# Kernel tuning notes

Hardware: AMD Instinct MI355X
Metric: run time of the kernel (lower is better)

## Reference

```python
import jax, jax.numpy as jnp
import numpy as np

IN_F, OUT_F, K, BATCH = 1024, 1024, 8, 4096


def setup_inputs() -> dict:
    key = jax.random.key(0)
    kx, ka, kb = jax.random.split(key, 3)
    x = jax.random.normal(kx, (BATCH, IN_F), dtype=jnp.float32)
    scale = 1.0 / (K * OUT_F)
    # a/b params: uniform in (-1,1)/(K*out_features), laid out [out, in, K]
    a = (2.0 * jax.random.uniform(ka, (OUT_F, IN_F, K)) - 1.0) * scale
    b = (2.0 * jax.random.uniform(kb, (OUT_F, IN_F, K)) - 1.0) * scale
    return {"x": x, "a": a.astype(jnp.float32), "b": b.astype(jnp.float32)}


def reference(x, a, b):
    # Fourier basis: k = 0..K-1 applied to every input feature
    K_ = a.shape[-1]
    ks = jnp.arange(K_, dtype=x.dtype)  # [K]
    phase = x[..., None] * ks  # [B, in, K]
    x_sin = jnp.sin(phase)
    x_cos = jnp.cos(phase)
    # y[b,o] = sum_{i,k} sin(k x_bi) a_oik + cos(k x_bi) b_oik
    y = jnp.einsum("bik,oik->bo", x_sin, a) + jnp.einsum("bik,oik->bo", x_cos, b)
    return y
```

## Files before the change

kernel.cpp:

```cpp
#include <hip/hip_runtime.h>

#define BATCH   4096
#define IN_F    1024
#define OUT_F   1024
#define KF      8
#define KD      14336

#define BM 256
#define BN 256
#define BK 64
#define KSPLIT 4
#define KCHUNK (KD/KSPLIT)
#define NT (KCHUNK/BK)
#define C_ELEMS ((size_t)BATCH * OUT_F)

#define QW 1040384.0f
#define DQ (1.0f/132128768.0f)

typedef int   i32x4 __attribute__((ext_vector_type(4)));
typedef float f32x4 __attribute__((ext_vector_type(4)));

__device__ __forceinline__ void gload_lds16(const void* g, void* l) {
  __builtin_amdgcn_global_load_lds((const __attribute__((address_space(1))) void*)g,
                                   (__attribute__((address_space(3))) void*)l,
                                   16, 0, 0);
}

__device__ __forceinline__ unsigned int pack4(int q0, int q1, int q2, int q3) {
  return (unsigned int)(q0 & 255) | ((unsigned int)(q1 & 255) << 8) |
         ((unsigned int)(q2 & 255) << 16) | ((unsigned int)(q3 & 255) << 24);
}

__global__ __launch_bounds__(256) void wconv_kernel(const float* __restrict__ a,
                                                    const float* __restrict__ b,
                                                    signed char* __restrict__ W,
                                                    float* __restrict__ bias) {
  const int o  = blockIdx.x;
  const int i0 = threadIdx.x * 4;
  const float4* ap = reinterpret_cast<const float4*>(a + (size_t)o * 8192 + i0 * 8);
  const float4* bp = reinterpret_cast<const float4*>(b + (size_t)o * 8192 + i0 * 8);
  union { float4 v[2]; float f[8]; } ua[4], ub[4];
#pragma unroll
  for (int ii = 0; ii < 4; ++ii) {
    ua[ii].v[0] = ap[2 * ii]; ua[ii].v[1] = ap[2 * ii + 1];
    ub[ii].v[0] = bp[2 * ii]; ub[ii].v[1] = bp[2 * ii + 1];
  }
  unsigned int* wp = reinterpret_cast<unsigned int*>(W + (size_t)o * KD + i0);
#pragma unroll
  for (int j = 0; j < 7; ++j) {
    int qa[4], qb[4];
#pragma unroll
    for (int ii = 0; ii < 4; ++ii) {
      qa[ii] = __float2int_rn(ua[ii].f[j + 1] * QW);
      qb[ii] = __float2int_rn(ub[ii].f[j + 1] * QW);
    }
    wp[j       * (IN_F / 4)] = pack4(qa[0], qa[1], qa[2], qa[3]);
    wp[(7 + j) * (IN_F / 4)] = pack4(qb[0], qb[1], qb[2], qb[3]);
  }
  float bsum = ub[0].f[0] + ub[1].f[0] + ub[2].f[0] + ub[3].f[0];
#pragma unroll
  for (int off = 32; off > 0; off >>= 1) bsum += __shfl_down(bsum, off);
  __shared__ float red[4];
  if ((threadIdx.x & 63) == 0) red[threadIdx.x >> 6] = bsum;
  __syncthreads();
  if (threadIdx.x == 0) bias[o] = red[0] + red[1] + red[2] + red[3];
}

__global__ __launch_bounds__(256) void feat_kernel(const float* __restrict__ x,
                                                   signed char* __restrict__ Xq) {
  int idx = blockIdx.x * 256 + threadIdx.x;
  int bb = idx >> 8;
  int i0 = (idx & 255) * 4;
  float4 xv = *reinterpret_cast<const float4*>(x + (size_t)bb * IN_F + i0);
  float sv[4][KF], cv[4][KF];
#pragma unroll
  for (int ii = 0; ii < 4; ++ii) {
    float xx = (ii == 0) ? xv.x : (ii == 1) ? xv.y : (ii == 2) ? xv.z : xv.w;
    sincosf(xx, &sv[ii][1], &cv[ii][1]);
#pragma unroll
    for (int k = 2; k < KF; ++k) {
      sv[ii][k] = sv[ii][k-1] * cv[ii][1] + cv[ii][k-1] * sv[ii][1];
      cv[ii][k] = cv[ii][k-1] * cv[ii][1] - sv[ii][k-1] * sv[ii][1];
    }
  }
  unsigned int* dst = reinterpret_cast<unsigned int*>(Xq + (size_t)bb * KD + i0);
#pragma unroll
  for (int j = 0; j < 7; ++j) {
    dst[j * (IN_F / 4)] = pack4(__float2int_rn(127.f * sv[0][j+1]), __float2int_rn(127.f * sv[1][j+1]),
                                __float2int_rn(127.f * sv[2][j+1]), __float2int_rn(127.f * sv[3][j+1]));
    dst[(7 + j) * (IN_F / 4)] = pack4(__float2int_rn(127.f * cv[0][j+1]), __float2int_rn(127.f * cv[1][j+1]),
                                      __float2int_rn(127.f * cv[2][j+1]), __float2int_rn(127.f * cv[3][j+1]));
  }
}

__global__ __launch_bounds__(512, 2) void gemm_kernel(const signed char* __restrict__ A,
                                                      const signed char* __restrict__ Bt,
                                                      int* __restrict__ Cout,
                                                      int use_slab) {
  __shared__ signed char sA[2][BM * BK];
  __shared__ signed char sB[2][BN * BK];

  const int tid  = threadIdx.x;
  const int wid  = tid >> 6;
  const int lane = tid & 63;
  const int wm = wid >> 2, wn = wid & 3;
  const int l15 = lane & 15;

  const int bid = blockIdx.x;
  const int s   = (bid & 7) * 32 + (bid >> 3);
  const int z   = s >> 6;
  const int mt  = s & 15;
  const int nt  = (s >> 4) & 3;
  const int m0  = mt * BM;
  const int n0  = nt * BN;
  const int fbase = z * KCHUNK;

  const int srow = wid * 16 + (lane >> 2);
  const int swz  = ((lane >> 2) & 3) ^ ((lane >> 4) & 3);
  const int gsrc = (lane & 3) ^ swz;
  const signed char* pA = A  + (size_t)(m0 + srow) * KD + fbase + gsrc * 16;
  const signed char* pB = Bt + (size_t)(n0 + srow) * KD + fbase + gsrc * 16;
  const int ldst = wid * 1024;

  const int rswz = (l15 & 3) ^ ((l15 >> 2) & 3);
  const int kgr  = (((lane >> 4) ^ rswz) & 3) * 16;
  const int arowb = (wm * 128 + l15) * BK;
  const int browb = (wn * 64 + l15) * BK;

  i32x4 acc[8][4] = {};
  i32x4 bfr[4];

#define PHASE(SAC, SBC, Q, STGP, STGDST, KOFF)                                  \
  {                                                                             \
    i32x4 af[4];                                                                \
    _Pragma("unroll") for (int f = 0; f < 4; ++f)                               \
      af[f] = *reinterpret_cast<const i32x4*>(                                  \
          (SAC) + arowb + ((Q) * 4 + f) * (16 * BK) + kgr);                     \
    if ((Q) == 0) {                                                             \
      _Pragma("unroll") for (int nf = 0; nf < 4; ++nf)                          \
        bfr[nf] = *reinterpret_cast<const i32x4*>(                              \
            (SBC) + browb + nf * (16 * BK) + kgr);                              \
    }                                                                           \
    gload_lds16((STGP) + (KOFF), (STGDST) + ldst);                              \
    gload_lds16((STGP) + (size_t)128 * KD + (KOFF), (STGDST) + 8192 + ldst);    \
    if ((Q) == 0) asm volatile("s_waitcnt lgkmcnt(4)" ::: "memory");            \
    asm volatile("s_barrier" ::: "memory");                                     \
    __builtin_amdgcn_s_setprio(1);                                              \
    _Pragma("unroll") for (int f = 0; f < 4; ++f)                               \
      _Pragma("unroll") for (int nf = 0; nf < 4; ++nf)                          \
        acc[(Q) * 4 + f][nf] = __builtin_amdgcn_mfma_i32_16x16x64_i8(           \
            af[f], bfr[nf], acc[(Q) * 4 + f][nf], 0, 0, 0);                     \
    __builtin_amdgcn_s_setprio(0);                                              \
    if ((Q) == 1) asm volatile("s_waitcnt vmcnt(2)" ::: "memory");              \
    asm volatile("s_barrier" ::: "memory");                                     \
  }

  gload_lds16(pA,                        &sA[0][ldst]);
  gload_lds16(pA + (size_t)128 * KD,     &sA[0][8192 + ldst]);
  gload_lds16(pB,                        &sB[0][ldst]);
  gload_lds16(pB + (size_t)128 * KD,     &sB[0][8192 + ldst]);
  gload_lds16(pB + BK,                   &sB[1][ldst]);
  gload_lds16(pB + (size_t)128 * KD + BK, &sB[1][8192 + ldst]);
  asm volatile("s_waitcnt vmcnt(2)" ::: "memory");
  asm volatile("s_barrier" ::: "memory");

  for (int j = 0; j < NT / 2; ++j) {
    const int kA1 = (2 * j + 1) * BK;
    const int kB2 = (2 * j + 2 < NT) ? (2 * j + 2) * BK : 0;
    const int kB3 = (2 * j + 3 < NT) ? (2 * j + 3) * BK : 0;

    PHASE(&sA[0][0], &sB[0][0], 0, pA, &sA[1][0], kA1)
    PHASE(&sA[0][0], &sB[0][0], 1, pB, &sB[0][0], kB2)
    PHASE(&sA[1][0], &sB[1][0], 0, pA, &sA[0][0], kB2)
    PHASE(&sA[1][0], &sB[1][0], 1, pB, &sB[1][0], kB3)
  }
#undef PHASE

  const int crow = m0 + wm * 128 + (lane >> 4) * 4;
  const int ccol = n0 + wn * 64 + l15;
  if (use_slab) {
    int* Cz = Cout + (size_t)z * C_ELEMS;
#pragma unroll
    for (int mf = 0; mf < 8; ++mf)
#pragma unroll
      for (int nf = 0; nf < 4; ++nf)
#pragma unroll
        for (int jj = 0; jj < 4; ++jj)
          Cz[(size_t)(crow + mf * 16 + jj) * OUT_F + ccol + nf * 16] = acc[mf][nf][jj];
  } else {
    float* Cf = reinterpret_cast<float*>(Cout);
#pragma unroll
    for (int mf = 0; mf < 8; ++mf)
#pragma unroll
      for (int nf = 0; nf < 4; ++nf)
#pragma unroll
        for (int jj = 0; jj < 4; ++jj)
          atomicAdd(&Cf[(size_t)(crow + mf * 16 + jj) * OUT_F + ccol + nf * 16],
                    (float)acc[mf][nf][jj] * DQ);
  }
}

__global__ __launch_bounds__(256) void reduce_kernel(const i32x4* __restrict__ s,
                                                     const float* __restrict__ bias,
                                                     f32x4* __restrict__ y) {
  size_t i = (size_t)blockIdx.x * 256 + threadIdx.x;
  const size_t NQ = C_ELEMS / 4;
  i32x4 v = s[i] + s[i + NQ] + s[i + 2 * NQ] + s[i + 3 * NQ];
  f32x4 bv = reinterpret_cast<const f32x4*>(bias)[i & 255];
  f32x4 r;
  r[0] = (float)v[0] * DQ + bv[0];
  r[1] = (float)v[1] * DQ + bv[1];
  r[2] = (float)v[2] * DQ + bv[2];
  r[3] = (float)v[3] * DQ + bv[3];
  y[i] = r;
}

__global__ __launch_bounds__(256) void binit_kernel(const float* __restrict__ bias,
                                                    f32x4* __restrict__ y) {
  size_t i = (size_t)blockIdx.x * 256 + threadIdx.x;
  y[i] = reinterpret_cast<const f32x4*>(bias)[i & 255];
}

__global__ __launch_bounds__(256) void naive_kernel(const float* __restrict__ x,
                                                    const float* __restrict__ a,
                                                    const float* __restrict__ b,
                                                    float* __restrict__ y) {
  int o  = blockIdx.x * 256 + threadIdx.x;
  int bb = blockIdx.y;
  __shared__ float xs[IN_F];
  for (int i = threadIdx.x; i < IN_F; i += 256) xs[i] = x[(size_t)bb * IN_F + i];
  __syncthreads();
  float acc = 0.f;
  for (int i = 0; i < IN_F; ++i) {
    float s1, c1; sincosf(xs[i], &s1, &c1);
    float sk = 0.f, ck = 1.f;
    const float* ap = a + (size_t)o * 8192 + i * KF;
    const float* bp = b + (size_t)o * 8192 + i * KF;
#pragma unroll
    for (int k = 0; k < KF; ++k) {
      acc += sk * ap[k] + ck * bp[k];
      float sn = sk * c1 + ck * s1;
      ck = ck * c1 - sk * s1;
      sk = sn;
    }
  }
  y[(size_t)bb * OUT_F + o] = acc;
}

extern "C" void kernel_launch(void* const* d_in, const int* in_sizes, int n_in,
                              void* d_out, int out_size, void* d_ws, size_t ws_size,
                              hipStream_t stream) {
  (void)in_sizes; (void)n_in; (void)out_size;
  const float* x = (const float*)d_in[0];
  const float* a = (const float*)d_in[1];
  const float* b = (const float*)d_in[2];
  float* y = (float*)d_out;

  const size_t XQ_BYTES   = (size_t)BATCH * KD;
  const size_t WQ_BYTES   = (size_t)OUT_F * KD;
  const size_t BIAS_BYTES = (size_t)OUT_F * sizeof(float);
  const size_t SLAB_BYTES = C_ELEMS * sizeof(int) * KSPLIT;

  if (ws_size >= XQ_BYTES + WQ_BYTES + BIAS_BYTES) {
    signed char* Xq = (signed char*)d_ws;
    signed char* Wq = (signed char*)d_ws + XQ_BYTES;
    float* bias     = (float*)((char*)d_ws + XQ_BYTES + WQ_BYTES);
    int* slabs      = (int*)((char*)d_ws + XQ_BYTES + WQ_BYTES + BIAS_BYTES);
    const bool slab = ws_size >= XQ_BYTES + WQ_BYTES + BIAS_BYTES + SLAB_BYTES;

    wconv_kernel<<<OUT_F, 256, 0, stream>>>(a, b, Wq, bias);
    feat_kernel<<<(BATCH * IN_F / 4) / 256, 256, 0, stream>>>(x, Xq);
    if (slab) {
      gemm_kernel<<<dim3((BATCH / BM) * (OUT_F / BN) * KSPLIT), 512, 0, stream>>>(Xq, Wq, slabs, 1);
      reduce_kernel<<<(int)(C_ELEMS / 4 / 256), 256, 0, stream>>>((const i32x4*)slabs, bias, (f32x4*)y);
    } else {
      binit_kernel<<<(int)(C_ELEMS / 4 / 256), 256, 0, stream>>>(bias, (f32x4*)y);
      gemm_kernel<<<dim3((BATCH / BM) * (OUT_F / BN) * KSPLIT), 512, 0, stream>>>(Xq, Wq, (int*)y, 0);
    }
  } else {
    naive_kernel<<<dim3(OUT_F / 256, BATCH), 256, 0, stream>>>(x, a, b, y);
  }
}
```

Measured before the change: 118.3 us.

## Load B fragments directly from global into registers, drop B LDS staging

Removes the shared-memory double buffer for the B operand. Each wave now loads its B fragments straight from global memory into registers, double-buffered across tiles. Only A is staged through LDS, which halves LDS traffic and footprint and changes the barrier schedule. The cost is that B fragments are no longer shared across the two M-waves that use them, so redundant global/L2 reads go up. Global latency is also exposed on the register path, and the __syncthreads at the end of each tile adds serialization.

Result: slower. 132.2 us (+11.7%).

```diff
diff --git a/kernel.cpp b/kernel.cpp
--- a/kernel.cpp
+++ b/kernel.cpp
@@ -98,7 +98,6 @@
                                                       int* __restrict__ Cout,
                                                       int use_slab) {
   __shared__ signed char sA[2][BM * BK];
-  __shared__ signed char sB[2][BN * BK];
 
   const int tid  = threadIdx.x;
   const int wid  = tid >> 6;
@@ -118,63 +117,65 @@
   const int srow = wid * 16 + (lane >> 2);
   const int swz  = ((lane >> 2) & 3) ^ ((lane >> 4) & 3);
   const int gsrc = (lane & 3) ^ swz;
-  const signed char* pA = A  + (size_t)(m0 + srow) * KD + fbase + gsrc * 16;
-  const signed char* pB = Bt + (size_t)(n0 + srow) * KD + fbase + gsrc * 16;
+  const signed char* pA = A + (size_t)(m0 + srow) * KD + fbase + gsrc * 16;
   const int ldst = wid * 1024;
 
   const int rswz = (l15 & 3) ^ ((l15 >> 2) & 3);
   const int kgr  = (((lane >> 4) ^ rswz) & 3) * 16;
   const int arowb = (wm * 128 + l15) * BK;
-  const int browb = (wn * 64 + l15) * BK;
+
+  const signed char* pBf = Bt + (size_t)(n0 + wn * 64 + l15) * KD + fbase + (lane >> 4) * 16;
 
   i32x4 acc[8][4] = {};
-  i32x4 bfr[4];
-
-#define PHASE(SAC, SBC, Q, STGP, STGDST, KOFF)                                  \
-  {                                                                             \
-    i32x4 af[4];                                                                \
-    _Pragma("unroll") for (int f = 0; f < 4; ++f)                               \
-      af[f] = *reinterpret_cast<const i32x4*>(                                  \
-          (SAC) + arowb + ((Q) * 4 + f) * (16 * BK) + kgr);                     \
-    if ((Q) == 0) {                                                             \
-      _Pragma("unroll") for (int nf = 0; nf < 4; ++nf)                          \
-        bfr[nf] = *reinterpret_cast<const i32x4*>(                              \
-            (SBC) + browb + nf * (16 * BK) + kgr);                              \
-    }                                                                           \
-    gload_lds16((STGP) + (KOFF), (STGDST) + ldst);                              \
-    gload_lds16((STGP) + (size_t)128 * KD + (KOFF), (STGDST) + 8192 + ldst);    \
-    if ((Q) == 0) asm volatile("s_waitcnt lgkmcnt(4)" ::: "memory");            \
-    asm volatile("s_barrier" ::: "memory");                                     \
-    __builtin_amdgcn_s_setprio(1);                                              \
-    _Pragma("unroll") for (int f = 0; f < 4; ++f)                               \
-      _Pragma("unroll") for (int nf = 0; nf < 4; ++nf)                          \
-        acc[(Q) * 4 + f][nf] = __builtin_amdgcn_mfma_i32_16x16x64_i8(           \
-            af[f], bfr[nf], acc[(Q) * 4 + f][nf], 0, 0, 0);                     \
-    __builtin_amdgcn_s_setprio(0);                                              \
-    if ((Q) == 1) asm volatile("s_waitcnt vmcnt(2)" ::: "memory");              \
-    asm volatile("s_barrier" ::: "memory");                                     \
-  }
-
-  gload_lds16(pA,                        &sA[0][ldst]);
-  gload_lds16(pA + (size_t)128 * KD,     &sA[0][8192 + ldst]);
-  gload_lds16(pB,                        &sB[0][ldst]);
-  gload_lds16(pB + (size_t)128 * KD,     &sB[0][8192 + ldst]);
-  gload_lds16(pB + BK,                   &sB[1][ldst]);
-  gload_lds16(pB + (size_t)128 * KD + BK, &sB[1][8192 + ldst]);
-  asm volatile("s_waitcnt vmcnt(2)" ::: "memory");
-  asm volatile("s_barrier" ::: "memory");
+  i32x4 BA[4], BB[4];
+
+#define TILE(SAC, SAN, BC, BN_, KOFF)                                          \
+  {                                                                            \
+    gload_lds16(pA + (KOFF), (SAN) + ldst);                                    \
+    gload_lds16(pA + (size_t)128 * KD + (KOFF), (SAN) + 8192 + ldst);          \
+    _Pragma("unroll") for (int nf = 0; nf < 4; ++nf)                           \
+      BN_[nf] = *reinterpret_cast<const i32x4*>(                               \
+          pBf + (size_t)nf * 16 * KD + (KOFF));                                \
+    __builtin_amdgcn_sched_barrier(0);                                         \
+    i32x4 af[8];                                                               \
+    _Pragma("unroll") for (int f = 0; f < 4; ++f)                              \
+      af[f] = *reinterpret_cast<const i32x4*>(                                 \
+          (SAC) + arowb + f * (16 * BK) + kgr);                                \
+    asm volatile("s_barrier" ::: "memory");                                    \
+    __builtin_amdgcn_s_setprio(1);                                             \
+    _Pragma("unroll") for (int f = 0; f < 4; ++f)                              \
+      _Pragma("unroll") for (int nf = 0; nf < 4; ++nf)                         \
+        acc[f][nf] = __builtin_amdgcn_mfma_i32_16x16x64_i8(                    \
+            af[f], BC[nf], acc[f][nf], 0, 0, 0);                               \
+    __builtin_amdgcn_s_setprio(0);                                             \
+    asm volatile("s_barrier" ::: "memory");                                    \
+    _Pragma("unroll") for (int f = 4; f < 8; ++f)                              \
+      af[f] = *reinterpret_cast<const i32x4*>(                                 \
+          (SAC) + arowb + f * (16 * BK) + kgr);                                \
+    asm volatile("s_barrier" ::: "memory");                                    \
+    __builtin_amdgcn_s_setprio(1);                                             \
+    _Pragma("unroll") for (int f = 4; f < 8; ++f)                              \
+      _Pragma("unroll") for (int nf = 0; nf < 4; ++nf)                         \
+        acc[f][nf] = __builtin_amdgcn_mfma_i32_16x16x64_i8(                    \
+            af[f], BC[nf], acc[f][nf], 0, 0, 0);                               \
+    __builtin_amdgcn_s_setprio(0);                                             \
+    __syncthreads();                                                           \
+  }
+
+  gload_lds16(pA, &sA[0][ldst]);
+  gload_lds16(pA + (size_t)128 * KD, &sA[0][8192 + ldst]);
+#pragma unroll
+  for (int nf = 0; nf < 4; ++nf)
+    BA[nf] = *reinterpret_cast<const i32x4*>(pBf + (size_t)nf * 16 * KD);
+  __syncthreads();
 
   for (int j = 0; j < NT / 2; ++j) {
-    const int kA1 = (2 * j + 1) * BK;
-    const int kB2 = (2 * j + 2 < NT) ? (2 * j + 2) * BK : 0;
-    const int kB3 = (2 * j + 3 < NT) ? (2 * j + 3) * BK : 0;
-
-    PHASE(&sA[0][0], &sB[0][0], 0, pA, &sA[1][0], kA1)
-    PHASE(&sA[0][0], &sB[0][0], 1, pB, &sB[0][0], kB2)
-    PHASE(&sA[1][0], &sB[1][0], 0, pA, &sA[0][0], kB2)
-    PHASE(&sA[1][0], &sB[1][0], 1, pB, &sB[1][0], kB3)
-  }
-#undef PHASE
+    const int k1 = (2 * j + 1) * BK;
+    const int k2 = (2 * j + 2 < NT) ? (2 * j + 2) * BK : 0;
+    TILE(&sA[0][0], &sA[1][0], BA, BB, k1)
+    TILE(&sA[1][0], &sA[0][0], BB, BA, k2)
+  }
+#undef TILE
 
   const int crow = m0 + wm * 128 + (lane >> 4) * 4;
   const int ccol = n0 + wn * 64 + l15;
```
